# Performance work log

Hardware: AMD Instinct MI355X
Metric: run time of the kernel (lower is better)

The kernel has to match this reference:

```python
import jax, jax.numpy as jnp
import numpy as np

N_NODES = 100000
N_EDGES = 3200000
ENTITY_DIM = 128
LAYER_DIMS = [128, 64, 32]


def setup_inputs() -> dict:
    key = jax.random.key(0)
    ks = jax.random.split(key, 20)
    inp = {
        "x": jax.random.normal(ks[0], (N_NODES, ENTITY_DIM), dtype=jnp.float32) * 0.1,
        "src_idx": jax.random.randint(ks[1], (N_EDGES,), 0, N_NODES, dtype=jnp.int32),
        "dst_idx": jax.random.randint(ks[2], (N_EDGES,), 0, N_NODES, dtype=jnp.int32),
        "edge_attn": jax.random.uniform(ks[3], (N_EDGES,), dtype=jnp.float32),
    }
    in_dim = ENTITY_DIM
    ki = 4
    for li, out_dim in enumerate(LAYER_DIMS):
        scale = jnp.sqrt(2.0 / (in_dim + out_dim)).astype(jnp.float32)
        inp[f"W1_{li}"] = jax.random.normal(ks[ki], (in_dim, out_dim), dtype=jnp.float32) * scale
        inp[f"b1_{li}"] = jnp.zeros((out_dim,), dtype=jnp.float32)
        inp[f"W2_{li}"] = jax.random.normal(ks[ki + 1], (in_dim, out_dim), dtype=jnp.float32) * scale
        inp[f"b2_{li}"] = jnp.zeros((out_dim,), dtype=jnp.float32)
        ki += 2
        in_dim = out_dim
    return inp


def _kgat_layer(x, src_idx, dst_idx, a, W1, b1, W2, b2):
    # edge-weighted sparse aggregation: h_n[v] = sum_{(u->v)} a_e * x[u]
    msgs = x[src_idx] * a[:, None]                       # [E, D] gather + scale
    h_n = jax.ops.segment_sum(msgs, dst_idx, num_segments=x.shape[0])  # [N, D]
    # bi-interaction fuse
    out = jax.nn.leaky_relu((x + h_n) @ W1 + b1) + jax.nn.leaky_relu((x * h_n) @ W2 + b2)
    return out


def reference(x, src_idx, dst_idx, edge_attn,
              W1_0, b1_0, W2_0, b2_0,
              W1_1, b1_1, W2_1, b2_1,
              W1_2, b1_2, W2_2, b2_2):
    params = [(W1_0, b1_0, W2_0, b2_0), (W1_1, b1_1, W2_1, b2_1), (W1_2, b1_2, W2_2, b2_2)]
    embs = [x]
    h = x
    for (W1, b1, W2, b2) in params:
        h = _kgat_layer(h, src_idx, dst_idx, edge_attn, W1, b1, W2, b2)
        embs.append(h)
    return jnp.concatenate(embs, axis=1)  # [N, 128+128+64+32]
```

## Files before the change

kernel.cpp:

```cpp
#include <hip/hip_runtime.h>
#include <hip/hip_bf16.h>

#define LRELU_SLOPE 0.01f

typedef __attribute__((ext_vector_type(8))) short short8;
typedef __attribute__((ext_vector_type(4))) float f32x4;

__device__ __forceinline__ unsigned int f2bf_rne(float f) {
    unsigned int u = __float_as_uint(f);
    u += 0x7FFFu + ((u >> 16) & 1u);
    return u >> 16;
}
__device__ __forceinline__ float bf_lo(unsigned int u) { return __uint_as_float(u << 16); }
__device__ __forceinline__ float bf_hi(unsigned int u) { return __uint_as_float(u & 0xFFFF0000u); }

__device__ __forceinline__ unsigned int pack_edge(int src, float a) {
    int q = (int)(a * 32767.0f + 0.5f);
    q = q < 0 ? 0 : (q > 32767 ? 32767 : q);
    return ((unsigned int)src << 15) | (unsigned int)q;
}

__global__ void bucket_count_kernel(const int* __restrict__ dst,
                                    int* __restrict__ bucket_total, int E, int NB) {
    __shared__ int cnt[512];
    const int t = threadIdx.x;
    const int tile0 = blockIdx.x * 8192;
    for (int i = t; i < 512; i += 256) cnt[i] = 0;
    __syncthreads();
#pragma unroll
    for (int j = 0; j < 32; ++j) {
        int e = tile0 + j * 256 + t;
        if (e < E) atomicAdd(&cnt[dst[e] >> 8], 1);
    }
    __syncthreads();
    for (int i = t; i < NB; i += 256) {
        int c = cnt[i];
        if (c) atomicAdd(&bucket_total[i], c);
    }
}

__global__ void bucket_scan_kernel(const int* __restrict__ bucket_total,
                                   int* __restrict__ bucket_base,
                                   int* __restrict__ row_ptr, int NB, int n) {
    __shared__ int s[512];
    const int t = threadIdx.x;
    int c = (t < NB) ? bucket_total[t] : 0;
    s[t] = c;
    __syncthreads();
    for (int off = 1; off < 512; off <<= 1) {
        int v = (t >= off) ? s[t - off] : 0;
        __syncthreads();
        s[t] += v;
        __syncthreads();
    }
    if (t < NB) bucket_base[t] = s[t] - c;
    if (t == 511) {
        bucket_base[NB] = s[511];
        row_ptr[n] = s[511];
    }
}

__global__ void bucket_scatter_kernel(const int* __restrict__ dst,
                                      const int* __restrict__ src,
                                      const float* __restrict__ attn,
                                      const int* __restrict__ bucket_base,
                                      int* __restrict__ bucket_fill,
                                      int2* __restrict__ bsa,
                                      int E, int NB) {
    __shared__ int cnt[512];
    __shared__ int basef[512];
    const int t = threadIdx.x;
    const int tile0 = blockIdx.x * 4096;
    for (int i = t; i < 512; i += 256) cnt[i] = 0;
    __syncthreads();
    int d[16], lr[16];
#pragma unroll
    for (int j = 0; j < 16; ++j) {
        int e = tile0 + j * 256 + t;
        if (e < E) {
            d[j] = dst[e];
            lr[j] = atomicAdd(&cnt[d[j] >> 8], 1);
        }
    }
    __syncthreads();
    for (int i = t; i < NB; i += 256) {
        int c = cnt[i];
        int r = c ? atomicAdd(&bucket_fill[i], c) : 0;
        basef[i] = bucket_base[i] + r;
    }
    __syncthreads();
#pragma unroll
    for (int j = 0; j < 16; ++j) {
        int e = tile0 + j * 256 + t;
        if (e < E) {
            int pos = basef[d[j] >> 8] + lr[j];
            unsigned int px = ((unsigned int)src[e] << 8) | (unsigned int)(d[j] & 255);
            bsa[pos] = make_int2((int)px, __float_as_int(attn[e]));
        }
    }
}

__global__ void bucket_build_kernel(const int* __restrict__ bucket_base,
                                    const int2* __restrict__ bsa,
                                    int* __restrict__ row_ptr,
                                    unsigned int* __restrict__ csr_pk,
                                    int n) {
    __shared__ int cnt[256];
    __shared__ int pre[256];
    __shared__ int cur[256];
    const int t = threadIdx.x;
    const int k = blockIdx.x;
    const int base = bucket_base[k];
    const int M = bucket_base[k + 1] - base;
    const int node0 = k << 8;
    if (t < 256) cnt[t] = 0;
    __syncthreads();
    for (int i = t; i < M; i += 1024)
        atomicAdd(&cnt[(unsigned int)bsa[base + i].x & 255u], 1);
    __syncthreads();
    if (t < 256) pre[t] = cnt[t];
    __syncthreads();
    for (int off = 1; off < 256; off <<= 1) {
        int v = (t < 256 && t >= off) ? pre[t - off] : 0;
        __syncthreads();
        if (t < 256) pre[t] += v;
        __syncthreads();
    }
    if (t < 256) {
        pre[t] -= cnt[t];
        cur[t] = pre[t];
        int dnode = node0 + t;
        if (dnode < n) row_ptr[dnode] = base + pre[t];
    }
    __syncthreads();
    for (int i = t; i < M; i += 1024) {
        int2 sa = bsa[base + i];
        unsigned int px = (unsigned int)sa.x;
        int local = (int)(px & 255u);
        int srcv  = (int)(px >> 8);
        int p = base + atomicAdd(&cur[local], 1);
        csr_pk[p] = pack_edge(srcv, __int_as_float(sa.y));
    }
}

__global__ void count_rank_kernel(const int* __restrict__ dst, int* __restrict__ counts,
                                  int* __restrict__ rank, int E) {
    const int base = blockIdx.x * (blockDim.x * 4) + threadIdx.x;
#pragma unroll
    for (int j = 0; j < 4; ++j) {
        int e = base + j * 256;
        if (e < E) rank[e] = atomicAdd(&counts[dst[e]], 1);
    }
}

__global__ void count_kernel(const int* __restrict__ dst, int* __restrict__ counts, int E) {
    int e = blockIdx.x * blockDim.x + threadIdx.x;
    if (e < E) atomicAdd(&counts[dst[e]], 1);
}

__global__ void scan_blocks_kernel(int* __restrict__ counts, int* __restrict__ row_ptr,
                                   int* __restrict__ partials, int n) {
    __shared__ int s[1024];
    const int t = threadIdx.x;
    const int i = blockIdx.x * 1024 + t;
    int c = (i < n) ? counts[i] : 0;
    s[t] = c;
    __syncthreads();
    for (int off = 1; off < 1024; off <<= 1) {
        int v = (t >= off) ? s[t - off] : 0;
        __syncthreads();
        s[t] += v;
        __syncthreads();
    }
    if (i < n) {
        row_ptr[i] = s[t] - c;
        counts[i] = 0;
    }
    if (t == 1023) partials[blockIdx.x] = s[1023];
}

__global__ void scan_partials_kernel(int* __restrict__ partials, int* __restrict__ row_ptr,
                                     int G, int n) {
    __shared__ int s[1024];
    const int t = threadIdx.x;
    int c = (t < G) ? partials[t] : 0;
    s[t] = c;
    __syncthreads();
    for (int off = 1; off < 1024; off <<= 1) {
        int v = (t >= off) ? s[t - off] : 0;
        __syncthreads();
        s[t] += v;
        __syncthreads();
    }
    if (t < G) partials[t] = s[t] - c;
    if (t == 1023) row_ptr[n] = s[1023];
}

__global__ void scan_add_kernel(int* __restrict__ row_ptr, const int* __restrict__ partials, int n) {
    int i = blockIdx.x * blockDim.x + threadIdx.x;
    if (i < n) row_ptr[i] += partials[i >> 10];
}

__global__ void fill_rank_kernel(const int* __restrict__ src, const int* __restrict__ dst,
                                 const float* __restrict__ attn,
                                 const int* __restrict__ row_ptr, const int* __restrict__ rank,
                                 unsigned int* __restrict__ csr_pk, int E) {
    const int base = blockIdx.x * (blockDim.x * 4) + threadIdx.x;
    int  e[4], d[4], r[4], s[4];
    float a[4];
    bool ok[4];
#pragma unroll
    for (int j = 0; j < 4; ++j) {
        e[j] = base + j * 256;
        ok[j] = e[j] < E;
        int idx = ok[j] ? e[j] : 0;
        d[j] = dst[idx];
        r[j] = rank[idx];
        s[j] = src[idx];
        a[j] = attn[idx];
    }
    int p[4];
#pragma unroll
    for (int j = 0; j < 4; ++j) p[j] = row_ptr[d[j]] + r[j];
#pragma unroll
    for (int j = 0; j < 4; ++j)
        if (ok[j]) csr_pk[p[j]] = pack_edge(s[j], a[j]);
}

__global__ void fill_kernel(const int* __restrict__ src, const int* __restrict__ dst,
                            const float* __restrict__ attn,
                            const int* __restrict__ row_ptr, int* __restrict__ counts,
                            int2* __restrict__ csr_edge, int E) {
    int e = blockIdx.x * blockDim.x + threadIdx.x;
    if (e < E) {
        int d = dst[e];
        int pos = row_ptr[d] + atomicAdd(&counts[d], 1);
        csr_edge[pos] = make_int2(src[e], __float_as_int(attn[e]));
    }
}

__global__ void copy_cvt_kernel(const float4* __restrict__ x, float4* __restrict__ out,
                                uint2* __restrict__ xb, int n4) {
    int i = blockIdx.x * blockDim.x + threadIdx.x;
    if (i < n4) {
        float4 v = x[i];
        int nd = i >> 5;
        int c = i & 31;
        out[(long)nd * 88 + c] = v;
        xb[i] = make_uint2(f2bf_rne(v.x) | (f2bf_rne(v.y) << 16),
                           f2bf_rne(v.z) | (f2bf_rne(v.w) << 16));
    }
}

__global__ void copy_x_kernel(const float4* __restrict__ x, float4* __restrict__ out, int n4) {
    int i = blockIdx.x * blockDim.x + threadIdx.x;
    if (i < n4) {
        int v = i >> 5;
        int c = i & 31;
        out[(long)v * 88 + c] = x[i];
    }
}

__global__ void wtrans_all_kernel(const float* __restrict__ W1_0, const float* __restrict__ W2_0,
                                  const float* __restrict__ W1_1, const float* __restrict__ W2_1,
                                  const float* __restrict__ W1_2, const float* __restrict__ W2_2,
                                  unsigned short* __restrict__ t10, unsigned short* __restrict__ t20,
                                  unsigned short* __restrict__ t11, unsigned short* __restrict__ t21,
                                  unsigned short* __restrict__ t12, unsigned short* __restrict__ t22) {
    int i = blockIdx.x * blockDim.x + threadIdx.x;
    const float* W; unsigned short* T; int in_d, out_d, base;
    if      (i < 16384) { W = W1_0; T = t10; in_d = 128; out_d = 128; base = 0; }
    else if (i < 32768) { W = W2_0; T = t20; in_d = 128; out_d = 128; base = 16384; }
    else if (i < 40960) { W = W1_1; T = t11; in_d = 128; out_d = 64;  base = 32768; }
    else if (i < 49152) { W = W2_1; T = t21; in_d = 128; out_d = 64;  base = 40960; }
    else if (i < 51200) { W = W1_2; T = t12; in_d = 64;  out_d = 32;  base = 49152; }
    else if (i < 53248) { W = W2_2; T = t22; in_d = 64;  out_d = 32;  base = 51200; }
    else return;
    int idx = i - base;
    int o = idx / in_d, k = idx - o * in_d;
    T[idx] = (unsigned short)f2bf_rne(W[(long)k * out_d + o]);
}

__global__ void agg128_bf_kernel(const unsigned int* __restrict__ xb,
                                 const int* __restrict__ row_ptr,
                                 const unsigned int* __restrict__ csr,
                                 unsigned int* __restrict__ hb, int n_nodes) {
    const int lane = threadIdx.x & 63;
    const int wid = (blockIdx.x * blockDim.x + threadIdx.x) >> 6;
    if (wid >= n_nodes) return;
    const int e0 = __builtin_amdgcn_readfirstlane(row_ptr[wid]);
    const int e1 = __builtin_amdgcn_readfirstlane(row_ptr[wid + 1]);
    float2 accA = {0.f, 0.f}, accB = {0.f, 0.f};
    int e = e0;
    for (; e + 8 <= e1; e += 8) {
        unsigned int px[8], u[8];
#pragma unroll
        for (int j = 0; j < 8; ++j) px[j] = csr[e + j];
#pragma unroll
        for (int j = 0; j < 8; ++j) u[j] = xb[(long)(px[j] >> 15) * 64 + lane];
#pragma unroll
        for (int j = 0; j < 8; ++j) {
            float q = (float)(px[j] & 32767u);
            if (j & 1) { accB.x = fmaf(q, bf_lo(u[j]), accB.x); accB.y = fmaf(q, bf_hi(u[j]), accB.y); }
            else       { accA.x = fmaf(q, bf_lo(u[j]), accA.x); accA.y = fmaf(q, bf_hi(u[j]), accA.y); }
        }
    }
    for (; e < e1; ++e) {
        unsigned int px = csr[e];
        unsigned int u = xb[(long)(px >> 15) * 64 + lane];
        float q = (float)(px & 32767u);
        accA.x = fmaf(q, bf_lo(u), accA.x); accA.y = fmaf(q, bf_hi(u), accA.y);
    }
    const float s = 1.0f / 32767.0f;
    float hx = (accA.x + accB.x) * s;
    float hy = (accA.y + accB.y) * s;
    hb[(long)wid * 64 + lane] = f2bf_rne(hx) | (f2bf_rne(hy) << 16);
}

__global__ void agg64_bf_kernel(const unsigned int* __restrict__ xb,
                                const int* __restrict__ row_ptr,
                                const unsigned int* __restrict__ csr,
                                unsigned int* __restrict__ hb, int n_nodes) {
    const int lane = threadIdx.x & 63;
    const int half = lane >> 5;
    const int l = lane & 31;
    const int wid = (blockIdx.x * blockDim.x + threadIdx.x) >> 6;
    if (wid >= n_nodes) return;
    const int e0 = __builtin_amdgcn_readfirstlane(row_ptr[wid]);
    const int e1 = __builtin_amdgcn_readfirstlane(row_ptr[wid + 1]);
    float2 accA = {0.f, 0.f}, accB = {0.f, 0.f};
    int e = e0;
    for (; e + 4 <= e1; e += 4) {
        unsigned int pA = csr[e + half];
        unsigned int pB = csr[e + 2 + half];
        unsigned int uA = xb[(long)(pA >> 15) * 32 + l];
        unsigned int uB = xb[(long)(pB >> 15) * 32 + l];
        float qA = (float)(pA & 32767u), qB = (float)(pB & 32767u);
        accA.x = fmaf(qA, bf_lo(uA), accA.x); accA.y = fmaf(qA, bf_hi(uA), accA.y);
        accB.x = fmaf(qB, bf_lo(uB), accB.x); accB.y = fmaf(qB, bf_hi(uB), accB.y);
    }
    if (e + 2 <= e1) {
        unsigned int p = csr[e + half];
        unsigned int u = xb[(long)(p >> 15) * 32 + l];
        float q = (float)(p & 32767u);
        accA.x = fmaf(q, bf_lo(u), accA.x); accA.y = fmaf(q, bf_hi(u), accA.y);
        e += 2;
    }
    if (e < e1 && half == 0) {
        unsigned int p = csr[e];
        unsigned int u = xb[(long)(p >> 15) * 32 + l];
        float q = (float)(p & 32767u);
        accA.x = fmaf(q, bf_lo(u), accA.x); accA.y = fmaf(q, bf_hi(u), accA.y);
    }
    accA.x += accB.x; accA.y += accB.y;
    accA.x += __shfl_xor(accA.x, 32);
    accA.y += __shfl_xor(accA.y, 32);
    if (half == 0) {
        const float s = 1.0f / 32767.0f;
        hb[(long)wid * 32 + l] = f2bf_rne(accA.x * s) | (f2bf_rne(accA.y * s) << 16);
    }
}

template <int D>
__global__ void agg_f32_kernel(const float* __restrict__ xin, long xstride,
                               const int* __restrict__ row_ptr,
                               const int2* __restrict__ csr_edge,
                               float* __restrict__ hagg, int n_nodes) {
    const int lane = threadIdx.x & 63;
    const int wid = (blockIdx.x * blockDim.x + threadIdx.x) >> 6;
    if (wid >= n_nodes) return;
    const int e0 = row_ptr[wid], e1 = row_ptr[wid + 1];
    if (D == 128) {
        float2 accA = {0.f, 0.f}, accB = {0.f, 0.f};
        int e = e0;
        for (; e + 2 <= e1; e += 2) {
            int2 p0 = csr_edge[e + 0];
            int2 p1 = csr_edge[e + 1];
            float2 x0 = reinterpret_cast<const float2*>(xin + (long)p0.x * xstride)[lane];
            float2 x1 = reinterpret_cast<const float2*>(xin + (long)p1.x * xstride)[lane];
            float a0 = __int_as_float(p0.y), a1 = __int_as_float(p1.y);
            accA.x = fmaf(a0, x0.x, accA.x); accA.y = fmaf(a0, x0.y, accA.y);
            accB.x = fmaf(a1, x1.x, accB.x); accB.y = fmaf(a1, x1.y, accB.y);
        }
        for (; e < e1; ++e) {
            int2 p = csr_edge[e];
            float2 xv = reinterpret_cast<const float2*>(xin + (long)p.x * xstride)[lane];
            float a = __int_as_float(p.y);
            accA.x = fmaf(a, xv.x, accA.x); accA.y = fmaf(a, xv.y, accA.y);
        }
        accA.x += accB.x; accA.y += accB.y;
        reinterpret_cast<float2*>(hagg + (long)wid * 128)[lane] = accA;
    } else {
        float accA = 0.f;
        for (int e = e0; e < e1; ++e) {
            int2 p = csr_edge[e];
            accA = fmaf(__int_as_float(p.y), xin[(long)p.x * xstride + lane], accA);
        }
        hagg[(long)wid * 64 + lane] = accA;
    }
}

template <int IN, int OUT>
__global__ __launch_bounds__(256) void mlp_mfma_kernel(
    const unsigned int* __restrict__ xin_bf,
    const unsigned int* __restrict__ hagg_bf,
    const unsigned short* __restrict__ W1T, const float* __restrict__ b1,
    const unsigned short* __restrict__ W2T, const float* __restrict__ b2,
    float* __restrict__ out, long ostride,
    unsigned short* __restrict__ xb_next, int n_nodes)
{
    constexpr int BM  = 64;
    constexpr int NCH = IN / 8;
    constexpr int KK  = IN / 32;
    constexpr int NT  = OUT / 16;
    constexpr int RU  = IN / 2;

    __shared__ uint4 xp_s[BM * NCH];
    __shared__ uint4 xm_s[BM * NCH];

    const int t = threadIdx.x;
    const int node0 = blockIdx.x * BM;

    for (int idx = t; idx < BM * NCH; idx += 256) {
        int n = idx / NCH;
        int c = idx - n * NCH;
        int v = node0 + n;
        uint4 xv = {0u,0u,0u,0u}, hv = {0u,0u,0u,0u};
        if (v < n_nodes) {
            xv = *reinterpret_cast<const uint4*>(xin_bf  + (long)v * RU + c * 4);
            hv = *reinterpret_cast<const uint4*>(hagg_bf + (long)v * RU + c * 4);
        }
        uint4 up, um;
        {
            float xl = bf_lo(xv.x), xh = bf_hi(xv.x), hl = bf_lo(hv.x), hh = bf_hi(hv.x);
            up.x = f2bf_rne(xl + hl) | (f2bf_rne(xh + hh) << 16);
            um.x = f2bf_rne(xl * hl) | (f2bf_rne(xh * hh) << 16);
        }
        {
            float xl = bf_lo(xv.y), xh = bf_hi(xv.y), hl = bf_lo(hv.y), hh = bf_hi(hv.y);
            up.y = f2bf_rne(xl + hl) | (f2bf_rne(xh + hh) << 16);
            um.y = f2bf_rne(xl * hl) | (f2bf_rne(xh * hh) << 16);
        }
        {
            float xl = bf_lo(xv.z), xh = bf_hi(xv.z), hl = bf_lo(hv.z), hh = bf_hi(hv.z);
            up.z = f2bf_rne(xl + hl) | (f2bf_rne(xh + hh) << 16);
            um.z = f2bf_rne(xl * hl) | (f2bf_rne(xh * hh) << 16);
        }
        {
            float xl = bf_lo(xv.w), xh = bf_hi(xv.w), hl = bf_lo(hv.w), hh = bf_hi(hv.w);
            up.w = f2bf_rne(xl + hl) | (f2bf_rne(xh + hh) << 16);
            um.w = f2bf_rne(xl * hl) | (f2bf_rne(xh * hh) << 16);
        }
        int sc = c ^ (n & 7);
        xp_s[n * NCH + sc] = up;
        xm_s[n * NCH + sc] = um;
    }
    __syncthreads();

    const int lane = t & 63;
    const int wv   = t >> 6;
    const int arow = lane & 15;
    const int kgrp = lane >> 4;
    const int lrow = wv * 16 + arow;

    short8 ap[KK], am[KK];
#pragma unroll
    for (int kk = 0; kk < KK; ++kk) {
        int c  = kk * 4 + kgrp;
        int sc = c ^ (lrow & 7);
        ap[kk] = *reinterpret_cast<const short8*>(&xp_s[lrow * NCH + sc]);
        am[kk] = *reinterpret_cast<const short8*>(&xm_s[lrow * NCH + sc]);
    }

    f32x4 acc1[NT], acc2[NT];
#pragma unroll
    for (int nt = 0; nt < NT; ++nt) {
        acc1[nt] = (f32x4){0.f, 0.f, 0.f, 0.f};
        acc2[nt] = (f32x4){0.f, 0.f, 0.f, 0.f};
    }

#pragma unroll
    for (int nt = 0; nt < NT; ++nt) {
        const long nb = (long)(nt * 16 + arow) * IN + kgrp * 8;
#pragma unroll
        for (int kk = 0; kk < KK; ++kk) {
            short8 bw1 = *reinterpret_cast<const short8*>(W1T + nb + kk * 32);
            acc1[nt] = __builtin_amdgcn_mfma_f32_16x16x32_bf16(ap[kk], bw1, acc1[nt], 0, 0, 0);
            short8 bw2 = *reinterpret_cast<const short8*>(W2T + nb + kk * 32);
            acc2[nt] = __builtin_amdgcn_mfma_f32_16x16x32_bf16(am[kk], bw2, acc2[nt], 0, 0, 0);
        }
    }

    const int mbase = node0 + wv * 16 + kgrp * 4;
#pragma unroll
    for (int nt = 0; nt < NT; ++nt) {
        int n = nt * 16 + arow;
        float bb1 = b1[n], bb2 = b2[n];
#pragma unroll
        for (int j = 0; j < 4; ++j) {
            int v = mbase + j;
            if (v < n_nodes) {
                float r1 = acc1[nt][j] + bb1;
                float r2 = acc2[nt][j] + bb2;
                r1 = r1 >= 0.f ? r1 : LRELU_SLOPE * r1;
                r2 = r2 >= 0.f ? r2 : LRELU_SLOPE * r2;
                float r = r1 + r2;
                out[(long)v * ostride + n] = r;
                if (xb_next) xb_next[(long)v * OUT + n] = (unsigned short)f2bf_rne(r);
            }
        }
    }
}

template <int IN, int OUT, int NT>
__global__ void mlp_kernel(const float* __restrict__ xin, long xstride,
                           const float* __restrict__ hagg,
                           const float* __restrict__ W1, const float* __restrict__ b1,
                           const float* __restrict__ W2, const float* __restrict__ b2,
                           float* __restrict__ out, long ostride,
                           unsigned short* __restrict__ xb_next, int n_nodes) {
    constexpr int SLOTS = 256 / OUT;
    constexpr int NPB = SLOTS * NT;
    __shared__ float s_xp[NPB][IN + 4];
    __shared__ float s_xm[NPB][IN + 4];
    const int t = threadIdx.x;
    const int o = t % OUT;
    const int slot = t / OUT;
    const int node0 = blockIdx.x * NPB;

    for (int idx = t; idx < NPB * (IN / 4); idx += 256) {
        int n = idx / (IN / 4), c = idx % (IN / 4);
        int k = c * 4;
        int v = node0 + n;
        float4 xv = {0.f, 0.f, 0.f, 0.f}, hv = {0.f, 0.f, 0.f, 0.f};
        if (v < n_nodes) {
            xv = *reinterpret_cast<const float4*>(xin + (long)v * xstride + k);
            hv = *reinterpret_cast<const float4*>(hagg + (long)v * IN + k);
        }
        *reinterpret_cast<float4*>(&s_xp[n][k]) =
            make_float4(xv.x + hv.x, xv.y + hv.y, xv.z + hv.z, xv.w + hv.w);
        *reinterpret_cast<float4*>(&s_xm[n][k]) =
            make_float4(xv.x * hv.x, xv.y * hv.y, xv.z * hv.z, xv.w * hv.w);
    }
    __syncthreads();

    float acc1[NT], acc2[NT];
#pragma unroll
    for (int j = 0; j < NT; ++j) { acc1[j] = 0.f; acc2[j] = 0.f; }

    for (int k = 0; k < IN; k += 4) {
        float w10 = W1[(k + 0) * OUT + o], w11 = W1[(k + 1) * OUT + o];
        float w12 = W1[(k + 2) * OUT + o], w13 = W1[(k + 3) * OUT + o];
        float w20 = W2[(k + 0) * OUT + o], w21 = W2[(k + 1) * OUT + o];
        float w22 = W2[(k + 2) * OUT + o], w23 = W2[(k + 3) * OUT + o];
#pragma unroll
        for (int j = 0; j < NT; ++j) {
            int n = slot * NT + j;
            float4 xp = *reinterpret_cast<const float4*>(&s_xp[n][k]);
            float4 xm = *reinterpret_cast<const float4*>(&s_xm[n][k]);
            acc1[j] = fmaf(xp.x, w10, acc1[j]); acc1[j] = fmaf(xp.y, w11, acc1[j]);
            acc1[j] = fmaf(xp.z, w12, acc1[j]); acc1[j] = fmaf(xp.w, w13, acc1[j]);
            acc2[j] = fmaf(xm.x, w20, acc2[j]); acc2[j] = fmaf(xm.y, w21, acc2[j]);
            acc2[j] = fmaf(xm.z, w22, acc2[j]); acc2[j] = fmaf(xm.w, w23, acc2[j]);
        }
    }

    const float bb1 = b1[o], bb2 = b2[o];
#pragma unroll
    for (int j = 0; j < NT; ++j) {
        int v = node0 + slot * NT + j;
        if (v < n_nodes) {
            float r1 = acc1[j] + bb1;
            float r2 = acc2[j] + bb2;
            r1 = r1 >= 0.f ? r1 : LRELU_SLOPE * r1;
            r2 = r2 >= 0.f ? r2 : LRELU_SLOPE * r2;
            float r = r1 + r2;
            out[(long)v * ostride + o] = r;
            if (xb_next) xb_next[(long)v * OUT + o] = (unsigned short)f2bf_rne(r);
        }
    }
}

extern "C" void kernel_launch(void* const* d_in, const int* in_sizes, int n_in,
                              void* d_out, int out_size, void* d_ws, size_t ws_size,
                              hipStream_t stream) {
    const float* x    = (const float*)d_in[0];
    const int*   src  = (const int*)d_in[1];
    const int*   dst  = (const int*)d_in[2];
    const float* attn = (const float*)d_in[3];
    const float* W1_0 = (const float*)d_in[4];
    const float* b1_0 = (const float*)d_in[5];
    const float* W2_0 = (const float*)d_in[6];
    const float* b2_0 = (const float*)d_in[7];
    const float* W1_1 = (const float*)d_in[8];
    const float* b1_1 = (const float*)d_in[9];
    const float* W2_1 = (const float*)d_in[10];
    const float* b2_1 = (const float*)d_in[11];
    const float* W1_2 = (const float*)d_in[12];
    const float* b1_2 = (const float*)d_in[13];
    const float* W2_2 = (const float*)d_in[14];
    const float* b2_2 = (const float*)d_in[15];
    float* out = (float*)d_out;

    const int N = in_sizes[0] / 128;
    const int E = in_sizes[1];

    char* w = (char*)d_ws;
    size_t off = 0;
    auto alloc = [&](size_t bytes) -> void* {
        void* p = w + off;
        off += (bytes + 511) & ~(size_t)511;
        return p;
    };
    int*          counts   = (int*)alloc((size_t)N * 4);
    int*          row_ptr  = (int*)alloc((size_t)(N + 1) * 4);
    int*          partials = (int*)alloc((size_t)1024 * 4);
    unsigned int* csr_pk   = (unsigned int*)alloc((size_t)E * 8);
    float*        h_agg    = (float*)alloc((size_t)N * 128 * 4);
    unsigned int* xb_a     = (unsigned int*)alloc((size_t)N * 128 * 2);
    unsigned int* xb_b     = (unsigned int*)alloc((size_t)N * 128 * 2);
    unsigned short* w1t0   = (unsigned short*)alloc((size_t)128 * 128 * 2);
    unsigned short* w2t0   = (unsigned short*)alloc((size_t)128 * 128 * 2);
    unsigned short* w1t1   = (unsigned short*)alloc((size_t)64 * 128 * 2);
    unsigned short* w2t1   = (unsigned short*)alloc((size_t)64 * 128 * 2);
    unsigned short* w1t2   = (unsigned short*)alloc((size_t)32 * 64 * 2);
    unsigned short* w2t2   = (unsigned short*)alloc((size_t)32 * 64 * 2);
    const bool use_bf16 = (off <= ws_size) && (N <= (1 << 17));

    const int NB = (N + 255) >> 8;
    int* bucket_mem  = (int*)alloc((size_t)2 * NB * 4);
    int* bucket_base = (int*)alloc((size_t)(NB + 1) * 4);
    const size_t off_fast = off;

    int2* bsa = (int2*)h_agg;
    const bool use_fast = use_bf16 && (off_fast <= ws_size) && (NB <= 512) &&
                          ((size_t)E * 8 <= (size_t)N * 512);

    int* rank = (int*)alloc((size_t)E * 4);
    const bool use_rank = use_bf16 && (off <= ws_size);

    const int G = (N + 1023) / 1024;
    unsigned int* h_bf = (unsigned int*)h_agg;

    if (use_fast) {
        int* bucket_total = bucket_mem;
        int* bucket_fill  = bucket_mem + NB;
        hipMemsetAsync(bucket_mem, 0, (size_t)2 * NB * 4, stream);
        bucket_count_kernel<<<(E + 8191) / 8192, 256, 0, stream>>>(dst, bucket_total, E, NB);
        bucket_scan_kernel<<<1, 512, 0, stream>>>(bucket_total, bucket_base, row_ptr, NB, N);
        bucket_scatter_kernel<<<(E + 4095) / 4096, 256, 0, stream>>>(
            dst, src, attn, bucket_base, bucket_fill, bsa, E, NB);
        bucket_build_kernel<<<NB, 1024, 0, stream>>>(bucket_base, bsa, row_ptr, csr_pk, N);
    } else if (use_bf16) {
        hipMemsetAsync(counts, 0, (size_t)N * 4, stream);
        if (use_rank) {
            count_rank_kernel<<<(E + 1023) / 1024, 256, 0, stream>>>(dst, counts, rank, E);
        } else {
            count_kernel<<<(E + 255) / 256, 256, 0, stream>>>(dst, counts, E);
        }
        scan_blocks_kernel<<<G, 1024, 0, stream>>>(counts, row_ptr, partials, N);
        scan_partials_kernel<<<1, 1024, 0, stream>>>(partials, row_ptr, G, N);
        scan_add_kernel<<<(N + 255) / 256, 256, 0, stream>>>(row_ptr, partials, N);
        if (use_rank) {
            fill_rank_kernel<<<(E + 1023) / 1024, 256, 0, stream>>>(src, dst, attn, row_ptr,
                                                                    rank, csr_pk, E);
        } else {
            fill_rank_kernel<<<(E + 1023) / 1024, 256, 0, stream>>>(src, dst, attn, row_ptr,
                                                                    rank, csr_pk, E);
        }
    } else {
        hipMemsetAsync(counts, 0, (size_t)N * 4, stream);
        count_kernel<<<(E + 255) / 256, 256, 0, stream>>>(dst, counts, E);
        scan_blocks_kernel<<<G, 1024, 0, stream>>>(counts, row_ptr, partials, N);
        scan_partials_kernel<<<1, 1024, 0, stream>>>(partials, row_ptr, G, N);
        scan_add_kernel<<<(N + 255) / 256, 256, 0, stream>>>(row_ptr, partials, N);
        fill_kernel<<<(E + 255) / 256, 256, 0, stream>>>(src, dst, attn, row_ptr, counts,
                                                         (int2*)csr_pk, E);
    }

    if (use_bf16) {
        copy_cvt_kernel<<<(N * 32 + 255) / 256, 256, 0, stream>>>(
            (const float4*)x, (float4*)out, (uint2*)xb_a, N * 32);
        wtrans_all_kernel<<<208, 256, 0, stream>>>(W1_0, W2_0, W1_1, W2_1, W1_2, W2_2,
                                                   w1t0, w2t0, w1t1, w2t1, w1t2, w2t2);

        agg128_bf_kernel<<<(N + 3) / 4, 256, 0, stream>>>(xb_a, row_ptr, csr_pk, h_bf, N);
        mlp_mfma_kernel<128, 128><<<(N + 63) / 64, 256, 0, stream>>>(
            xb_a, h_bf, w1t0, b1_0, w2t0, b2_0,
            out + 128, 352, (unsigned short*)xb_b, N);
        agg128_bf_kernel<<<(N + 3) / 4, 256, 0, stream>>>(xb_b, row_ptr, csr_pk, h_bf, N);
        mlp_mfma_kernel<128, 64><<<(N + 63) / 64, 256, 0, stream>>>(
            xb_b, h_bf, w1t1, b1_1, w2t1, b2_1,
            out + 256, 352, (unsigned short*)xb_a, N);
        agg64_bf_kernel<<<(N + 3) / 4, 256, 0, stream>>>(xb_a, row_ptr, csr_pk, h_bf, N);
        mlp_mfma_kernel<64, 32><<<(N + 63) / 64, 256, 0, stream>>>(
            xb_a, h_bf, w1t2, b1_2, w2t2, b2_2,
            out + 320, 352, (unsigned short*)nullptr, N);
    } else {
        copy_x_kernel<<<(N * 32 + 255) / 256, 256, 0, stream>>>((const float4*)x, (float4*)out, N * 32);
        agg_f32_kernel<128><<<(N + 3) / 4, 256, 0, stream>>>(x, 128, row_ptr, (const int2*)csr_pk, h_agg, N);
        mlp_kernel<128, 128, 4><<<(N + 7) / 8, 256, 0, stream>>>(x, 128, h_agg,
                                                                 W1_0, b1_0, W2_0, b2_0,
                                                                 out + 128, 352,
                                                                 (unsigned short*)nullptr, N);
        agg_f32_kernel<128><<<(N + 3) / 4, 256, 0, stream>>>(out + 128, 352, row_ptr, (const int2*)csr_pk, h_agg, N);
        mlp_kernel<128, 64, 4><<<(N + 15) / 16, 256, 0, stream>>>(out + 128, 352, h_agg,
                                                                  W1_1, b1_1, W2_1, b2_1,
                                                                  out + 256, 352,
                                                                  (unsigned short*)nullptr, N);
        agg_f32_kernel<64><<<(N + 3) / 4, 256, 0, stream>>>(out + 256, 352, row_ptr, (const int2*)csr_pk, h_agg, N);
        mlp_kernel<64, 32, 4><<<(N + 31) / 32, 256, 0, stream>>>(out + 256, 352, h_agg,
                                                                 W1_2, b1_2, W2_2, b2_2,
                                                                 out + 320, 352,
                                                                 (unsigned short*)nullptr, N);
    }
}
```

Measured before the change: 802.4 us.

## Sub-sort CSR edges within each row by coarse source-node block

The bucket build kernel now counts and scatters edges into 8 source-range sub-bins per destination row, so each row's edges are ordered by coarse source id. This is meant to improve locality of the x[src] gathers during aggregation across the three layers. The cost is larger shared-memory histograms and a 1024-wide scan in place of a 256-wide one. The non-fast path loses redundant branches, which is cleanup only.

```diff
diff --git a/kernel.cpp b/kernel.cpp
--- a/kernel.cpp
+++ b/kernel.cpp
@@ -104,33 +104,45 @@
                                     const int2* __restrict__ bsa,
                                     int* __restrict__ row_ptr,
                                     unsigned int* __restrict__ csr_pk,
-                                    int n) {
-    __shared__ int cnt[256];
-    __shared__ int pre[256];
-    __shared__ int cur[256];
+                                    int n, int sshift) {
+    __shared__ int cnt[2048];
+    __shared__ int pre[2048];
+    __shared__ int cur[2048];
+    __shared__ int ps[1024];
     const int t = threadIdx.x;
     const int k = blockIdx.x;
     const int base = bucket_base[k];
     const int M = bucket_base[k + 1] - base;
     const int node0 = k << 8;
-    if (t < 256) cnt[t] = 0;
-    __syncthreads();
-    for (int i = t; i < M; i += 1024)
-        atomicAdd(&cnt[(unsigned int)bsa[base + i].x & 255u], 1);
-    __syncthreads();
-    if (t < 256) pre[t] = cnt[t];
-    __syncthreads();
-    for (int off = 1; off < 256; off <<= 1) {
-        int v = (t < 256 && t >= off) ? pre[t - off] : 0;
+    cnt[t] = 0; cnt[t + 1024] = 0;
+    __syncthreads();
+    for (int i = t; i < M; i += 1024) {
+        int2 sa = bsa[base + i];
+        unsigned int px = (unsigned int)sa.x;
+        int local = (int)(px & 255u);
+        int blk = (int)(px >> 8) >> sshift; blk = blk > 7 ? 7 : blk;
+        atomicAdd(&cnt[(local << 3) | blk], 1);
+    }
+    __syncthreads();
+    int a = cnt[2 * t], b = cnt[2 * t + 1];
+    int pair = a + b;
+    ps[t] = pair;
+    __syncthreads();
+    for (int off = 1; off < 1024; off <<= 1) {
+        int v = (t >= off) ? ps[t - off] : 0;
         __syncthreads();
-        if (t < 256) pre[t] += v;
+        ps[t] += v;
         __syncthreads();
     }
+    int pbase = ps[t] - pair;
+    pre[2 * t]     = pbase;
+    pre[2 * t + 1] = pbase + a;
+    cur[2 * t]     = pbase;
+    cur[2 * t + 1] = pbase + a;
+    __syncthreads();
     if (t < 256) {
-        pre[t] -= cnt[t];
-        cur[t] = pre[t];
         int dnode = node0 + t;
-        if (dnode < n) row_ptr[dnode] = base + pre[t];
+        if (dnode < n) row_ptr[dnode] = base + pre[t << 3];
     }
     __syncthreads();
     for (int i = t; i < M; i += 1024) {
@@ -138,7 +150,8 @@
         unsigned int px = (unsigned int)sa.x;
         int local = (int)(px & 255u);
         int srcv  = (int)(px >> 8);
-        int p = base + atomicAdd(&cur[local], 1);
+        int blk = srcv >> sshift; blk = blk > 7 ? 7 : blk;
+        int p = base + atomicAdd(&cur[(local << 3) | blk], 1);
         csr_pk[p] = pack_edge(srcv, __int_as_float(sa.y));
     }
 }
@@ -642,6 +655,9 @@
     const int G = (N + 1023) / 1024;
     unsigned int* h_bf = (unsigned int*)h_agg;
 
+    int sshift = 0;
+    while (((N - 1) >> sshift) > 7) ++sshift;
+
     if (use_fast) {
         int* bucket_total = bucket_mem;
         int* bucket_fill  = bucket_mem + NB;
@@ -650,24 +666,15 @@
         bucket_scan_kernel<<<1, 512, 0, stream>>>(bucket_total, bucket_base, row_ptr, NB, N);
         bucket_scatter_kernel<<<(E + 4095) / 4096, 256, 0, stream>>>(
             dst, src, attn, bucket_base, bucket_fill, bsa, E, NB);
-        bucket_build_kernel<<<NB, 1024, 0, stream>>>(bucket_base, bsa, row_ptr, csr_pk, N);
+        bucket_build_kernel<<<NB, 1024, 0, stream>>>(bucket_base, bsa, row_ptr, csr_pk, N, sshift);
     } else if (use_bf16) {
         hipMemsetAsync(counts, 0, (size_t)N * 4, stream);
-        if (use_rank) {
-            count_rank_kernel<<<(E + 1023) / 1024, 256, 0, stream>>>(dst, counts, rank, E);
-        } else {
-            count_kernel<<<(E + 255) / 256, 256, 0, stream>>>(dst, counts, E);
-        }
+        count_rank_kernel<<<(E + 1023) / 1024, 256, 0, stream>>>(dst, counts, rank, E);
         scan_blocks_kernel<<<G, 1024, 0, stream>>>(counts, row_ptr, partials, N);
         scan_partials_kernel<<<1, 1024, 0, stream>>>(partials, row_ptr, G, N);
         scan_add_kernel<<<(N + 255) / 256, 256, 0, stream>>>(row_ptr, partials, N);
-        if (use_rank) {
-            fill_rank_kernel<<<(E + 1023) / 1024, 256, 0, stream>>>(src, dst, attn, row_ptr,
-                                                                    rank, csr_pk, E);
-        } else {
-            fill_rank_kernel<<<(E + 1023) / 1024, 256, 0, stream>>>(src, dst, attn, row_ptr,
-                                                                    rank, csr_pk, E);
-        }
+        fill_rank_kernel<<<(E + 1023) / 1024, 256, 0, stream>>>(src, dst, attn, row_ptr,
+                                                                rank, csr_pk, E);
     } else {
         hipMemsetAsync(counts, 0, (size_t)N * 4, stream);
         count_kernel<<<(E + 255) / 256, 256, 0, stream>>>(dst, counts, E);
```

Measured after the change: 806.3 us. Within noise of the previous version (+0.5%).
